# Performance work log

Hardware: AMD Instinct MI355X
Metric: run time of the kernel (lower is better)

The kernel has to match this reference:

```python
import jax, jax.numpy as jnp
import numpy as np

N_QUBITS = 4
DIM = 16
N_QLAYERS = 2

def _cnot_perm(c, t):
    idx = np.arange(DIM)
    cbit = (idx >> (N_QUBITS - 1 - c)) & 1
    return np.where(cbit == 1, idx ^ (1 << (N_QUBITS - 1 - t)), idx)

# ring entanglement: CNOT(0,1), CNOT(1,2), CNOT(2,3), CNOT(3,0)
RING_PERMS = [jnp.asarray(_cnot_perm(i, (i + 1) % N_QUBITS)) for i in range(N_QUBITS)]
_idx = np.arange(DIM)
ZSIGNS = jnp.asarray(np.stack([1.0 - 2.0 * ((_idx >> (N_QUBITS - 1 - q)) & 1) for q in range(N_QUBITS)], axis=1).astype(np.float32))  # (16, 4)

def _rx(t):
    c = jnp.cos(t / 2).astype(jnp.complex64)
    s = jnp.sin(t / 2).astype(jnp.complex64)
    return jnp.stack([jnp.stack([c, -1j * s]), jnp.stack([-1j * s, c])])

def _ry(t):
    c = jnp.cos(t / 2).astype(jnp.complex64)
    s = jnp.sin(t / 2).astype(jnp.complex64)
    return jnp.stack([jnp.stack([c, -s]), jnp.stack([s, c])])

def _rz(t):
    e = jnp.exp(-0.5j * t.astype(jnp.complex64))
    z = jnp.zeros((), jnp.complex64)
    return jnp.stack([jnp.stack([e, z]), jnp.stack([z, jnp.conj(e)])])

def _apply_1q(state, g, q):
    # wire 0 is the most significant bit (PennyLane convention)
    s = state.reshape(2 ** q, 2, 2 ** (N_QUBITS - 1 - q))
    return jnp.einsum('ij,ajc->aic', g, s).reshape(DIM)

def _circuit(angles, qw):
    # angles: (4,), qw: (n_qlayers, 4, 3); returns PauliZ expvals (4,)
    state = jnp.zeros(DIM, jnp.complex64).at[0].set(1.0)
    for q in range(N_QUBITS):
        state = _apply_1q(state, _ry(angles[q]), q)
    for l in range(N_QLAYERS):
        for q in range(N_QUBITS):
            state = _apply_1q(state, _rx(qw[l, q, 0]), q)
            state = _apply_1q(state, _ry(qw[l, q, 1]), q)
            state = _apply_1q(state, _rz(qw[l, q, 2]), q)
        for p in RING_PERMS:
            state = state[p]
    probs = jnp.abs(state) ** 2
    return probs @ ZSIGNS

def _conv(x, w, b, stride, pad):
    y = jax.lax.conv_general_dilated(x, w, (stride, stride), [(pad, pad), (pad, pad)], dimension_numbers=('NCHW', 'OIHW', 'NCHW'))
    return y + b[None, :, None, None]

def _bn(x, g, b, m, v):
    scale = (g / jnp.sqrt(v + 1e-5))[None, :, None, None]
    return (x - m[None, :, None, None]) * scale + b[None, :, None, None]

def _forward(x, c1w, c1b, bn1g, bn1b, bn1m, bn1v, c2w, c2b, bn2g, bn2b, bn2m, bn2v, c3w, c3b, bn3g, bn3b, bn3m, bn3v, pre_w, pre_b, qw, pw1, pb1, pw2, pb2):
    B = x.shape[0]
    h = jax.nn.relu(_bn(_conv(x, c1w, c1b, 4, 3), bn1g, bn1b, bn1m, bn1v))   # (B,32,56,56)
    h = jax.nn.relu(_bn(_conv(h, c2w, c2b, 2, 1), bn2g, bn2b, bn2m, bn2v))   # (B,64,28,28)
    h = jax.nn.relu(_bn(_conv(h, c3w, c3b, 2, 1), bn3g, bn3b, bn3m, bn3v))   # (B,128,14,14)
    h = h.reshape(B, 128, 2, 7, 2, 7).mean(axis=(3, 5))                       # AdaptiveAvgPool2d((2,2))
    f = h.reshape(B, 128 * 4)
    ang = jnp.tanh(f @ pre_w.T + pre_b) * jnp.pi                              # (B,4)
    qout = jax.vmap(lambda a: _circuit(a, qw))(ang)                            # (B,4) batched statevector sim
    h1 = jax.nn.relu(qout @ pw1.T + pb1)                                       # dropout inactive (eval)
    return h1 @ pw2.T + pb2

def setup_inputs() -> dict:
    key = jax.random.key(0)
    ks = jax.random.split(key, 16)
    d = {
        'x': jax.random.normal(ks[0], (128, 3, 224, 224), jnp.float32),
        'c1w': jax.random.normal(ks[1], (32, 3, 7, 7), jnp.float32) * 0.05,
        'c1b': jax.random.normal(ks[2], (32,), jnp.float32) * 0.05,
        'bn1g': jnp.ones((32,), jnp.float32), 'bn1b': jnp.zeros((32,), jnp.float32),
        'bn1m': jnp.zeros((32,), jnp.float32), 'bn1v': jnp.ones((32,), jnp.float32),
        'c2w': jax.random.normal(ks[3], (64, 32, 3, 3), jnp.float32) * 0.05,
        'c2b': jax.random.normal(ks[4], (64,), jnp.float32) * 0.05,
        'bn2g': jnp.ones((64,), jnp.float32), 'bn2b': jnp.zeros((64,), jnp.float32),
        'bn2m': jnp.zeros((64,), jnp.float32), 'bn2v': jnp.ones((64,), jnp.float32),
        'c3w': jax.random.normal(ks[5], (128, 64, 3, 3), jnp.float32) * 0.05,
        'c3b': jax.random.normal(ks[6], (128,), jnp.float32) * 0.05,
        'bn3g': jnp.ones((128,), jnp.float32), 'bn3b': jnp.zeros((128,), jnp.float32),
        'bn3m': jnp.zeros((128,), jnp.float32), 'bn3v': jnp.ones((128,), jnp.float32),
        'pre_w': jax.random.normal(ks[7], (4, 512), jnp.float32) * 0.04,
        'pre_b': jax.random.normal(ks[8], (4,), jnp.float32) * 0.04,
        'qw': jax.random.normal(ks[9], (2, 4, 3), jnp.float32) * 0.1,
        'pw1': jax.random.normal(ks[10], (64, 4), jnp.float32) * 0.5,
        'pb1': jax.random.normal(ks[11], (64,), jnp.float32) * 0.5,
        'pw2': jax.random.normal(ks[12], (5, 64), jnp.float32) * 0.12,
        'pb2': jax.random.normal(ks[13], (5,), jnp.float32) * 0.12,
    }
    return d

def reference(x, c1w, c1b, bn1g, bn1b, bn1m, bn1v, c2w, c2b, bn2g, bn2b, bn2m, bn2v, c3w, c3b, bn3g, bn3b, bn3m, bn3v, pre_w, pre_b, qw, pw1, pb1, pw2, pb2):
    return _forward(x, c1w, c1b, bn1g, bn1b, bn1m, bn1v, c2w, c2b, bn2g, bn2b, bn2m, bn2v, c3w, c3b, bn3g, bn3b, bn3m, bn3v, pre_w, pre_b, qw, pw1, pb1, pw2, pb2)
```

## Files before the change

### kernel.cpp

```cpp
#include <hip/hip_runtime.h>
#include <math.h>

#define DEV __device__ __forceinline__

typedef __attribute__((ext_vector_type(8))) __bf16 bf16x8;
typedef __attribute__((ext_vector_type(4))) float f32x4;

__global__ void prep_weights(
    const float* __restrict__ c1w, const float* __restrict__ c1b,
    const float* __restrict__ g1, const float* __restrict__ b1,
    const float* __restrict__ m1, const float* __restrict__ v1,
    const float* __restrict__ c2w, const float* __restrict__ c2b,
    const float* __restrict__ g2, const float* __restrict__ b2,
    const float* __restrict__ m2, const float* __restrict__ v2,
    const float* __restrict__ c3w, const float* __restrict__ c3b,
    const float* __restrict__ g3, const float* __restrict__ b3,
    const float* __restrict__ m3, const float* __restrict__ v3,
    __bf16* __restrict__ wb1, __bf16* __restrict__ wb2, __bf16* __restrict__ wb3,
    float* __restrict__ sc1, float* __restrict__ sh1,
    float* __restrict__ sc2, float* __restrict__ sh2,
    float* __restrict__ sc3, float* __restrict__ sh3)
{
    int gid = blockIdx.x * 256 + threadIdx.x;
    int gs = gridDim.x * 256;
    for (int e = gid; e < 32 * 192; e += gs) {
        int oc = e / 192, k = e % 192, rr = k >> 3, kw = k & 7;
        wb1[e] = (rr < 21 && kw >= 1) ? (__bf16)c1w[oc * 147 + rr * 7 + kw - 1]
                                      : (__bf16)0.f;
    }
    for (int e = gid; e < 64 * 384; e += gs) {
        int oc = e / 384, k = e % 384, rr = k >> 2, kw = k & 3;
        wb2[e] = (kw >= 1) ? (__bf16)c2w[oc * 288 + rr * 3 + kw - 1] : (__bf16)0.f;
    }
    for (int e = gid; e < 128 * 768; e += gs) {
        int oc = e / 768, k = e % 768, rr = k >> 2, kw = k & 3;
        wb3[e] = (kw >= 1) ? (__bf16)c3w[oc * 576 + rr * 3 + kw - 1] : (__bf16)0.f;
    }
    if (gid < 32) {
        float s = g1[gid] * rsqrtf(v1[gid] + 1e-5f);
        sc1[gid] = s; sh1[gid] = (c1b[gid] - m1[gid]) * s + b1[gid];
    } else if (gid < 96) {
        int i = gid - 32;
        float s = g2[i] * rsqrtf(v2[i] + 1e-5f);
        sc2[i] = s; sh2[i] = (c2b[i] - m2[i]) * s + b2[i];
    } else if (gid < 224) {
        int i = gid - 96;
        float s = g3[i] * rsqrtf(v3[i] + 1e-5f);
        sc3[i] = s; sh3[i] = (c3b[i] - m3[i]) * s + b3[i];
    }
}

__global__ __launch_bounds__(256, 3) void conv1_kernel(
    const float* __restrict__ x,
    const __bf16* __restrict__ wb,
    const float* __restrict__ scale, const float* __restrict__ shift,
    __bf16* __restrict__ out)
{
    constexpr int IHW = 224 * 224, OHW = 56 * 56, LDR = 72;
    __shared__ __attribute__((aligned(16))) __bf16 Is[256 * LDR];
    __shared__ __attribute__((aligned(16))) __bf16 Ws[32 * LDR];

    const int tid = threadIdx.x;
    const int sb0 = blockIdx.x * 256;
    const int sm = tid;

    int a_n, a_ih0, a_iw0;
    {
        int m = sb0 + sm;
        a_n = m / OHW;
        int rem = m % OHW;
        a_ih0 = (rem / 56) * 4 - 3;
        a_iw0 = (rem % 56) * 4 - 3;
    }
    unsigned ihok = 0;
    #pragma unroll
    for (int t = 0; t < 7; ++t)
        ihok |= (unsigned)(((a_ih0 + t) >= 0) && ((a_ih0 + t) < 224)) << t;
    const bool left = (a_iw0 < 0);
    const int boff = a_n * 3 * IHW + a_ih0 * 224 + (a_iw0 - 1);

    const int w_oc = tid >> 3, w_j = tid & 7;
    const int wave = tid >> 6, lane = tid & 63;
    const int quad = lane >> 4, l16 = lane & 15;

    f32x4 acc[2][4] = {};

    float4 RA[8], RB[8];
    bf16x8 wv;

    auto LOADI = [&](int ci) {
        #pragma unroll
        for (int r = 0; r < 8; ++r) {
            const int rr = ci * 8 + r;
            if (rr < 21) {
                const int ic = rr / 7, kh = rr % 7;
                int off = boff + (ic * IHW + kh * 224);
                int o0 = off < 0 ? 0 : off;
                int o1 = (off + 4) < 0 ? 0 : (off + 4);
                RA[r] = *(const float4*)(x + o0);
                RB[r] = *(const float4*)(x + o1);
            }
        }
        wv = *(const bf16x8*)&wb[(size_t)w_oc * 192 + ci * 64 + w_j * 8];
    };

    LOADI(0);

    #pragma unroll
    for (int ci = 0; ci < 3; ++ci) {
        __builtin_amdgcn_s_barrier();
        #pragma unroll
        for (int r = 0; r < 8; ++r) {
            const int rr = ci * 8 + r;
            bf16x8 h;
            if (rr >= 21) {
                h = (bf16x8){};
            } else {
                const int kh = rr % 7;
                float va[8] = {RA[r].x, RA[r].y, RA[r].z, RA[r].w,
                               RB[r].x, RB[r].y, RB[r].z, RB[r].w};
                bool rok = (ihok >> kh) & 1u;
                #pragma unroll
                for (int j = 0; j < 8; ++j) va[j] = rok ? va[j] : 0.f;
                #pragma unroll
                for (int j = 1; j <= 3; ++j) va[j] = left ? 0.f : va[j];
                #pragma unroll
                for (int j = 0; j < 8; ++j) h[j] = (__bf16)va[j];
            }
            *(bf16x8*)&Is[sm * LDR + r * 8] = h;
        }
        *(bf16x8*)&Ws[w_oc * LDR + w_j * 8] = wv;
        if (ci + 1 < 3) LOADI(ci + 1);
        asm volatile("s_waitcnt lgkmcnt(0)" ::: "memory");
        __builtin_amdgcn_s_barrier();

        #pragma unroll
        for (int kk = 0; kk < 2; ++kk) {
            bf16x8 afr[2], bfr[4];
            #pragma unroll
            for (int mt = 0; mt < 2; ++mt)
                afr[mt] = *(const bf16x8*)&Ws[(mt * 16 + l16) * LDR + kk * 32 + quad * 8];
            #pragma unroll
            for (int nt = 0; nt < 4; ++nt)
                bfr[nt] = *(const bf16x8*)&Is[(wave * 64 + nt * 16 + l16) * LDR + kk * 32 + quad * 8];
            #pragma unroll
            for (int mt = 0; mt < 2; ++mt)
                #pragma unroll
                for (int nt = 0; nt < 4; ++nt)
                    acc[mt][nt] = __builtin_amdgcn_mfma_f32_16x16x32_bf16(
                        afr[mt], bfr[nt], acc[mt][nt], 0, 0, 0);
        }
    }

    #pragma unroll
    for (int mt = 0; mt < 2; ++mt) {
        #pragma unroll
        for (int r = 0; r < 4; ++r) {
            int oc = mt * 16 + quad * 4 + r;
            float scl = scale[oc], shf = shift[oc];
            #pragma unroll
            for (int nt = 0; nt < 4; ++nt) {
                int sg = sb0 + wave * 64 + nt * 16 + l16;
                int n = sg / OHW, s = sg % OHW;
                float v = fmaf(acc[mt][nt][r], scl, shf);
                v = v > 0.f ? v : 0.f;
                out[((size_t)n * 32 + oc) * OHW + s] = (__bf16)v;
            }
        }
    }
}

template<int NOCT, int IC, int IH, int IW, int OH, int OW, int OC,
         int KTP, int KCH, int GXS>
DEV void conv_body64(
    const __bf16* __restrict__ xo,
    const __bf16* __restrict__ wb,
    const float* __restrict__ scale, const float* __restrict__ shift,
    __bf16* __restrict__ out, __bf16* Is, __bf16* Ws)
{
    constexpr int KS = 3, S = 2, P = 1;
    constexpr int KITER = KCH / 64;
    constexpr int OHW = OH * OW;
    constexpr int IHW = IH * IW;
    constexpr int LDR = 72;
    constexpr int WLD = NOCT / 2;

    const int tid = threadIdx.x;
    int bx = blockIdx.x;
    if (GXS > 0) bx = (bx & 7) * GXS + (bx >> 3);
    const int sb0 = bx * 256;
    const int oc0 = blockIdx.y * (NOCT * 16);

    const int sm = tid;
    int a_n, a_ih0, a_iw0;
    {
        int m = sb0 + sm;
        a_n = m / OHW;
        int rem = m % OHW;
        a_ih0 = (rem / OW) * S - P;
        a_iw0 = (rem % OW) * S - P;
    }
    unsigned ihok = 0;
    #pragma unroll
    for (int t = 0; t < KS; ++t)
        ihok |= (unsigned)(((a_ih0 + t) >= 0) && ((a_ih0 + t) < IH)) << t;
    const bool left = (a_iw0 < 0);
    const __bf16* xp = xo + ((size_t)a_n * IC * IHW + (ptrdiff_t)a_ih0 * IW
                             + (a_iw0 - 1));

    const int wave = tid >> 6, lane = tid & 63;
    const int quad = lane >> 4, l16 = lane & 15;

    f32x4 acc[NOCT][4] = {};

    unsigned Pu[32];
    bf16x8 wv[WLD];

    auto LOADI = [&](int ci) {
        const int k0 = ci * 64;
        #pragma unroll
        for (int r = 0; r < 16; ++r) {
            const int rr = (k0 / 4) + r;
            const int ic = rr / KS, kh = rr % KS;
            const unsigned* rp = (const unsigned*)(xp + (ic * IHW + kh * IW));
            Pu[r * 2]     = rp[0];
            Pu[r * 2 + 1] = rp[1];
        }
        #pragma unroll
        for (int i = 0; i < WLD; ++i) {
            int e = i * 256 + tid;
            wv[i] = *(const bf16x8*)&wb[(size_t)(oc0 + (e >> 3)) * KTP + k0 + (e & 7) * 8];
        }
    };

    LOADI(0);

    #pragma unroll
    for (int ci = 0; ci < KITER; ++ci) {
        __builtin_amdgcn_s_barrier();
        #pragma unroll
        for (int q = 0; q < 8; ++q) {
            union { unsigned u[4]; bf16x8 v; } tm;
            #pragma unroll
            for (int h = 0; h < 2; ++h) {
                const int r = 2 * q + h;
                const int kh = (ci * 16 + r) % KS;
                unsigned t0 = Pu[r * 2], t1 = Pu[r * 2 + 1];
                bool rok = (ihok >> kh) & 1u;
                t0 = rok ? t0 : 0u;
                t1 = rok ? t1 : 0u;
                t0 = left ? (t0 & 0x0000FFFFu) : t0;
                tm.u[h * 2]     = t0;
                tm.u[h * 2 + 1] = t1;
            }
            *(bf16x8*)&Is[sm * LDR + q * 8] = tm.v;
        }
        #pragma unroll
        for (int i = 0; i < WLD; ++i) {
            int e = i * 256 + tid;
            *(bf16x8*)&Ws[(e >> 3) * LDR + (e & 7) * 8] = wv[i];
        }
        if (ci + 1 < KITER) LOADI(ci + 1);
        asm volatile("s_waitcnt lgkmcnt(0)" ::: "memory");
        __builtin_amdgcn_s_barrier();

        #pragma unroll
        for (int kk = 0; kk < 2; ++kk) {
            bf16x8 afr[NOCT], bfr[4];
            #pragma unroll
            for (int mt = 0; mt < NOCT; ++mt)
                afr[mt] = *(const bf16x8*)&Ws[(mt * 16 + l16) * LDR + kk * 32 + quad * 8];
            #pragma unroll
            for (int nt = 0; nt < 4; ++nt)
                bfr[nt] = *(const bf16x8*)&Is[(wave * 64 + nt * 16 + l16) * LDR + kk * 32 + quad * 8];
            #pragma unroll
            for (int mt = 0; mt < NOCT; ++mt)
                #pragma unroll
                for (int nt = 0; nt < 4; ++nt)
                    acc[mt][nt] = __builtin_amdgcn_mfma_f32_16x16x32_bf16(
                        afr[mt], bfr[nt], acc[mt][nt], 0, 0, 0);
        }
    }

    #pragma unroll
    for (int mt = 0; mt < NOCT; ++mt) {
        #pragma unroll
        for (int r = 0; r < 4; ++r) {
            int oc = oc0 + mt * 16 + quad * 4 + r;
            float scl = scale[oc], shf = shift[oc];
            #pragma unroll
            for (int nt = 0; nt < 4; ++nt) {
                int sg = sb0 + wave * 64 + nt * 16 + l16;
                int n = sg / OHW, s = sg % OHW;
                float v = fmaf(acc[mt][nt][r], scl, shf);
                v = v > 0.f ? v : 0.f;
                out[((size_t)n * OC + oc) * OHW + s] = (__bf16)v;
            }
        }
    }
}

__global__ __launch_bounds__(256, 3) void conv2_kernel(
    const __bf16* __restrict__ xo, const __bf16* __restrict__ wb,
    const float* __restrict__ scale, const float* __restrict__ shift,
    __bf16* __restrict__ out)
{
    __shared__ __attribute__((aligned(16))) __bf16 Is[256 * 72];
    __shared__ __attribute__((aligned(16))) __bf16 Ws[64 * 72];
    conv_body64<4, 32, 56, 56, 28, 28, 64, 384, 384, 49>(
        xo, wb, scale, shift, out, Is, Ws);
}

__global__ __launch_bounds__(256, 3) void conv3_kernel(
    const __bf16* __restrict__ xo, const __bf16* __restrict__ wb,
    const float* __restrict__ scale, const float* __restrict__ shift,
    __bf16* __restrict__ out)
{
    __shared__ __attribute__((aligned(16))) __bf16 Is[256 * 72];
    __shared__ __attribute__((aligned(16))) __bf16 Ws[32 * 72];
    conv_body64<2, 64, 28, 28, 14, 14, 128, 768, 768, 0>(
        xo, wb, scale, shift, out, Is, Ws);
}

__global__ __launch_bounds__(256) void head_kernel(
    const __bf16* __restrict__ c3o,
    const float* __restrict__ pre_w, const float* __restrict__ pre_b,
    const float* __restrict__ qw,
    const float* __restrict__ pw1, const float* __restrict__ pb1,
    const float* __restrict__ pw2, const float* __restrict__ pb2,
    float* __restrict__ out)
{
    __shared__ __attribute__((aligned(16))) __bf16 slab[128 * 196];
    __shared__ float f[512];
    __shared__ float ang[4];
    __shared__ float zexp[4];
    __shared__ float h1[64];

    int b = blockIdx.x;
    int t = threadIdx.x;

    {
        const bf16x8* src = (const bf16x8*)(c3o + (size_t)b * 128 * 196);
        bf16x8* dst = (bf16x8*)slab;
        #pragma unroll
        for (int i = 0; i < 13; ++i) {
            int e = t + i * 256;
            if (e < 3136) dst[e] = src[e];
        }
    }
    __syncthreads();

    for (int p = t; p < 512; p += 256) {
        int c = p >> 2, i = (p >> 1) & 1, j = p & 1;
        int base = c * 196 + (i * 7) * 14 + j * 7;
        float s = 0.f;
        #pragma unroll
        for (int u = 0; u < 7; ++u)
            #pragma unroll
            for (int v = 0; v < 7; ++v)
                s += (float)slab[base + u * 14 + v];
        f[p] = s * (1.f / 49.f);
    }
    __syncthreads();

    int wv = t >> 6, lane = t & 63;
    float partial = 0.f;
    for (int d = lane; d < 512; d += 64)
        partial += f[d] * pre_w[wv * 512 + d];
    #pragma unroll
    for (int off = 32; off > 0; off >>= 1)
        partial += __shfl_down(partial, off, 64);
    if (lane == 0)
        ang[wv] = tanhf(partial + pre_b[wv]) * 3.14159265358979323846f;
    __syncthreads();

    if (t < 16) {
        const int i = t;
        float re = (i == 0) ? 1.f : 0.f;
        float im = 0.f;

        #pragma unroll
        for (int q = 0; q < 4; ++q) {
            const int m = 8 >> q;
            float th = ang[q] * 0.5f;
            float c = cosf(th), s = sinf(th);
            float pr = __shfl_xor(re, m, 64);
            float pi = __shfl_xor(im, m, 64);
            float ts = (i & m) ? s : -s;
            re = c * re + ts * pr;
            im = c * im + ts * pi;
        }
        #pragma unroll
        for (int l = 0; l < 2; ++l) {
            #pragma unroll
            for (int q = 0; q < 4; ++q) {
                const int m = 8 >> q;
                const float* qq = qw + (l * 4 + q) * 3;
                {
                    float th = qq[0] * 0.5f;
                    float c = cosf(th), s = sinf(th);
                    float pr = __shfl_xor(re, m, 64);
                    float pi = __shfl_xor(im, m, 64);
                    float rn = c * re + s * pi;
                    im = c * im - s * pr;
                    re = rn;
                }
                {
                    float th = qq[1] * 0.5f;
                    float c = cosf(th), s = sinf(th);
                    float pr = __shfl_xor(re, m, 64);
                    float pi = __shfl_xor(im, m, 64);
                    float ts = (i & m) ? s : -s;
                    re = c * re + ts * pr;
                    im = c * im + ts * pi;
                }
                {
                    float th = qq[2] * 0.5f;
                    float c = cosf(th), s = sinf(th);
                    float ts = (i & m) ? s : -s;
                    float rn = c * re - ts * im;
                    im = c * im + ts * re;
                    re = rn;
                }
            }
            #pragma unroll
            for (int e = 0; e < 4; ++e) {
                const int cm = 8 >> e, tm = 8 >> ((e + 1) & 3);
                float pr = __shfl_xor(re, tm, 64);
                float pi = __shfl_xor(im, tm, 64);
                bool sw = (i & cm) != 0;
                re = sw ? pr : re;
                im = sw ? pi : im;
            }
        }
        float p2 = re * re + im * im;
        #pragma unroll
        for (int q = 0; q < 4; ++q) {
            const int m = 8 >> q;
            float v = (i & m) ? -p2 : p2;
            v += __shfl_xor(v, 1, 64);
            v += __shfl_xor(v, 2, 64);
            v += __shfl_xor(v, 4, 64);
            v += __shfl_xor(v, 8, 64);
            if (i == 0) zexp[q] = v;
        }
    }
    __syncthreads();

    if (t < 64) {
        float s = pb1[t];
        #pragma unroll
        for (int k = 0; k < 4; ++k) s += zexp[k] * pw1[t * 4 + k];
        h1[t] = s > 0.f ? s : 0.f;
    }
    __syncthreads();

    if (t < 5) {
        float s = pb2[t];
        for (int k = 0; k < 64; ++k) s += h1[k] * pw2[t * 64 + k];
        out[b * 5 + t] = s;
    }
}

extern "C" void kernel_launch(void* const* d_in, const int* in_sizes, int n_in,
                              void* d_out, int out_size, void* d_ws, size_t ws_size,
                              hipStream_t stream) {
    const float* x    = (const float*)d_in[0];
    const float* c1w  = (const float*)d_in[1];
    const float* c1b  = (const float*)d_in[2];
    const float* bn1g = (const float*)d_in[3];
    const float* bn1b = (const float*)d_in[4];
    const float* bn1m = (const float*)d_in[5];
    const float* bn1v = (const float*)d_in[6];
    const float* c2w  = (const float*)d_in[7];
    const float* c2b  = (const float*)d_in[8];
    const float* bn2g = (const float*)d_in[9];
    const float* bn2b = (const float*)d_in[10];
    const float* bn2m = (const float*)d_in[11];
    const float* bn2v = (const float*)d_in[12];
    const float* c3w  = (const float*)d_in[13];
    const float* c3bi = (const float*)d_in[14];
    const float* bn3g = (const float*)d_in[15];
    const float* bn3b = (const float*)d_in[16];
    const float* bn3m = (const float*)d_in[17];
    const float* bn3v = (const float*)d_in[18];
    const float* prw  = (const float*)d_in[19];
    const float* prb  = (const float*)d_in[20];
    const float* qw   = (const float*)d_in[21];
    const float* pw1  = (const float*)d_in[22];
    const float* pb1  = (const float*)d_in[23];
    const float* pw2  = (const float*)d_in[24];
    const float* pb2  = (const float*)d_in[25];

    const int N = in_sizes[0] / (3 * 224 * 224);
    const size_t NC1 = (size_t)N * 32 * 56 * 56;
    const size_t NC2 = (size_t)N * 64 * 28 * 28;
    const size_t NC3 = (size_t)N * 128 * 14 * 14;

    __bf16* ws_h = (__bf16*)d_ws;
    __bf16* c1o = ws_h + 64;
    __bf16* c2o = ws_h + 64 + NC1 + 64 + 64;
    __bf16* c3o = ws_h + 64 + NC1 + 64 + 64 + NC2 + 64;
    __bf16* wb1 = c3o + NC3;
    __bf16* wb2 = wb1 + 32 * 192;
    __bf16* wb3 = wb2 + 64 * 384;
    float* sc1 = (float*)(wb3 + 128 * 768);
    float* sh1 = sc1 + 32;
    float* sc2 = sh1 + 32;  float* sh2 = sc2 + 64;
    float* sc3 = sh2 + 64;  float* sh3 = sc3 + 128;

    prep_weights<<<192, 256, 0, stream>>>(
        c1w, c1b, bn1g, bn1b, bn1m, bn1v,
        c2w, c2b, bn2g, bn2b, bn2m, bn2v,
        c3w, c3bi, bn3g, bn3b, bn3m, bn3v,
        wb1, wb2, wb3, sc1, sh1, sc2, sh2, sc3, sh3);

    conv1_kernel<<<dim3(401408 / 256, 1), 256, 0, stream>>>(x, wb1, sc1, sh1, c1o);
    conv2_kernel<<<dim3(100352 / 256, 1), 256, 0, stream>>>(c1o, wb2, sc2, sh2, c2o);
    conv3_kernel<<<dim3(25088 / 256, 4), 256, 0, stream>>>(c2o, wb3, sc3, sh3, c3o);
    head_kernel<<<N, 256, 0, stream>>>(c3o, prw, prb, qw,
                                       pw1, pb1, pw2, pb2, (float*)d_out);
}
```

Before: 231.6 us.

## Retile conv2/conv3 with smaller spatial blocks, cooperative row loads, and two-deep prefetch

The shared conv body is rewritten so each block covers fewer output positions (128 for conv2, 64 for conv3). Waves are split across output channels and spatial positions, and several threads share the im2col row loads for each position. Global loads are prefetched two K-steps ahead using alternating register sets, issued after the LDS barrier. The aim is more blocks for occupancy and more latency hiding, at the cost of extra weight reloads per block and more register pressure.

Measured after the change: 223.6 us. 3.5% less time.

```diff
diff --git a/kernel.cpp b/kernel.cpp
--- a/kernel.cpp
+++ b/kernel.cpp
@@ -170,9 +170,9 @@
     }
 }
 
-template<int NOCT, int IC, int IH, int IW, int OH, int OW, int OC,
-         int KTP, int KCH, int GXS>
-DEV void conv_body64(
+template<int SPB, int WSP, int IC, int IH, int IW, int OH, int OW, int OC,
+         int KCH, int GXS>
+DEV void conv_bodyB(
     const __bf16* __restrict__ xo,
     const __bf16* __restrict__ wb,
     const float* __restrict__ scale, const float* __restrict__ shift,
@@ -180,21 +180,25 @@
 {
     constexpr int KS = 3, S = 2, P = 1;
     constexpr int KITER = KCH / 64;
-    constexpr int OHW = OH * OW;
-    constexpr int IHW = IH * IW;
+    constexpr int OHW = OH * OW, IHW = IH * IW;
     constexpr int LDR = 72;
-    constexpr int WLD = NOCT / 2;
+    constexpr int TPS = 256 / SPB;
+    constexpr int RPT = 16 / TPS;
+    constexpr int WOC = 4 / WSP;
+    constexpr int WLD = (WOC * 32) / 32;
+    static_assert(KITER % 2 == 0, "double-buffer needs even KITER");
 
     const int tid = threadIdx.x;
     int bx = blockIdx.x;
     if (GXS > 0) bx = (bx & 7) * GXS + (bx >> 3);
-    const int sb0 = bx * 256;
-    const int oc0 = blockIdx.y * (NOCT * 16);
-
-    const int sm = tid;
+    const int sb0 = bx * SPB;
+
+    const int s_sp = tid & (SPB - 1);
+    const int gbase = (tid / SPB) * RPT;
+
     int a_n, a_ih0, a_iw0;
     {
-        int m = sb0 + sm;
+        int m = sb0 + s_sp;
         a_n = m / OHW;
         int rem = m % OHW;
         a_ih0 = (rem / OW) * S - P;
@@ -210,42 +214,43 @@
 
     const int wave = tid >> 6, lane = tid & 63;
     const int quad = lane >> 4, l16 = lane & 15;
-
-    f32x4 acc[NOCT][4] = {};
-
-    unsigned Pu[32];
-    bf16x8 wv[WLD];
-
-    auto LOADI = [&](int ci) {
+    const int woc = wave / WSP, wsp = wave - woc * WSP;
+
+    f32x4 acc[2][4] = {};
+
+    unsigned PuA[RPT * 2], PuB[RPT * 2];
+    bf16x8 wvA[WLD], wvB[WLD];
+
+    auto LOADI = [&](int ci, auto& Pu, auto& wv) {
         const int k0 = ci * 64;
         #pragma unroll
-        for (int r = 0; r < 16; ++r) {
-            const int rr = (k0 / 4) + r;
-            const int ic = rr / KS, kh = rr % KS;
-            const unsigned* rp = (const unsigned*)(xp + (ic * IHW + kh * IW));
-            Pu[r * 2]     = rp[0];
-            Pu[r * 2 + 1] = rp[1];
+        for (int j = 0; j < RPT; ++j) {
+            int rrr = ci * 16 + gbase + j;
+            unsigned ic = ((unsigned)rrr * 43691u) >> 17;
+            int kh = rrr - (int)ic * 3;
+            const unsigned* rp = (const unsigned*)(xp + ((int)ic * IHW + kh * IW));
+            Pu[j * 2]     = rp[0];
+            Pu[j * 2 + 1] = rp[1];
         }
         #pragma unroll
         for (int i = 0; i < WLD; ++i) {
             int e = i * 256 + tid;
-            wv[i] = *(const bf16x8*)&wb[(size_t)(oc0 + (e >> 3)) * KTP + k0 + (e & 7) * 8];
+            wv[i] = *(const bf16x8*)&wb[(size_t)(e >> 3) * KCH + k0 + (e & 7) * 8];
         }
     };
 
-    LOADI(0);
-
-    #pragma unroll
-    for (int ci = 0; ci < KITER; ++ci) {
+    auto STEP = [&](int ci, auto& Pu, auto& wv, auto& Pun, auto& wvn) {
         __builtin_amdgcn_s_barrier();
         #pragma unroll
-        for (int q = 0; q < 8; ++q) {
+        for (int q = 0; q < RPT / 2; ++q) {
             union { unsigned u[4]; bf16x8 v; } tm;
             #pragma unroll
             for (int h = 0; h < 2; ++h) {
-                const int r = 2 * q + h;
-                const int kh = (ci * 16 + r) % KS;
-                unsigned t0 = Pu[r * 2], t1 = Pu[r * 2 + 1];
+                const int j = 2 * q + h;
+                int rrr = ci * 16 + gbase + j;
+                unsigned icq = ((unsigned)rrr * 43691u) >> 17;
+                int kh = rrr - (int)icq * 3;
+                unsigned t0 = Pu[j * 2], t1 = Pu[j * 2 + 1];
                 bool rok = (ihok >> kh) & 1u;
                 t0 = rok ? t0 : 0u;
                 t1 = rok ? t1 : 0u;
@@ -253,44 +258,52 @@
                 tm.u[h * 2]     = t0;
                 tm.u[h * 2 + 1] = t1;
             }
-            *(bf16x8*)&Is[sm * LDR + q * 8] = tm.v;
+            *(bf16x8*)&Is[s_sp * LDR + (gbase + 2 * q) * 4] = tm.v;
         }
         #pragma unroll
         for (int i = 0; i < WLD; ++i) {
             int e = i * 256 + tid;
             *(bf16x8*)&Ws[(e >> 3) * LDR + (e & 7) * 8] = wv[i];
         }
-        if (ci + 1 < KITER) LOADI(ci + 1);
         asm volatile("s_waitcnt lgkmcnt(0)" ::: "memory");
         __builtin_amdgcn_s_barrier();
+        if (ci + 2 < KITER) LOADI(ci + 2, Pun, wvn);
 
         #pragma unroll
         for (int kk = 0; kk < 2; ++kk) {
-            bf16x8 afr[NOCT], bfr[4];
-            #pragma unroll
-            for (int mt = 0; mt < NOCT; ++mt)
-                afr[mt] = *(const bf16x8*)&Ws[(mt * 16 + l16) * LDR + kk * 32 + quad * 8];
+            bf16x8 afr[2], bfr[4];
+            #pragma unroll
+            for (int mt = 0; mt < 2; ++mt)
+                afr[mt] = *(const bf16x8*)&Ws[(woc * 32 + mt * 16 + l16) * LDR + kk * 32 + quad * 8];
             #pragma unroll
             for (int nt = 0; nt < 4; ++nt)
-                bfr[nt] = *(const bf16x8*)&Is[(wave * 64 + nt * 16 + l16) * LDR + kk * 32 + quad * 8];
-            #pragma unroll
-            for (int mt = 0; mt < NOCT; ++mt)
+                bfr[nt] = *(const bf16x8*)&Is[(wsp * 64 + nt * 16 + l16) * LDR + kk * 32 + quad * 8];
+            #pragma unroll
+            for (int mt = 0; mt < 2; ++mt)
                 #pragma unroll
                 for (int nt = 0; nt < 4; ++nt)
                     acc[mt][nt] = __builtin_amdgcn_mfma_f32_16x16x32_bf16(
                         afr[mt], bfr[nt], acc[mt][nt], 0, 0, 0);
         }
-    }
-
-    #pragma unroll
-    for (int mt = 0; mt < NOCT; ++mt) {
+    };
+
+    LOADI(0, PuA, wvA);
+    LOADI(1, PuB, wvB);
+    #pragma unroll
+    for (int cc = 0; cc < KITER; cc += 2) {
+        STEP(cc,     PuA, wvA, PuA, wvA);
+        STEP(cc + 1, PuB, wvB, PuB, wvB);
+    }
+
+    #pragma unroll
+    for (int mt = 0; mt < 2; ++mt) {
         #pragma unroll
         for (int r = 0; r < 4; ++r) {
-            int oc = oc0 + mt * 16 + quad * 4 + r;
+            int oc = woc * 32 + mt * 16 + quad * 4 + r;
             float scl = scale[oc], shf = shift[oc];
             #pragma unroll
             for (int nt = 0; nt < 4; ++nt) {
-                int sg = sb0 + wave * 64 + nt * 16 + l16;
+                int sg = sb0 + wsp * 64 + nt * 16 + l16;
                 int n = sg / OHW, s = sg % OHW;
                 float v = fmaf(acc[mt][nt][r], scl, shf);
                 v = v > 0.f ? v : 0.f;
@@ -305,9 +318,9 @@
     const float* __restrict__ scale, const float* __restrict__ shift,
     __bf16* __restrict__ out)
 {
-    __shared__ __attribute__((aligned(16))) __bf16 Is[256 * 72];
+    __shared__ __attribute__((aligned(16))) __bf16 Is[128 * 72];
     __shared__ __attribute__((aligned(16))) __bf16 Ws[64 * 72];
-    conv_body64<4, 32, 56, 56, 28, 28, 64, 384, 384, 49>(
+    conv_bodyB<128, 2, 32, 56, 56, 28, 28, 64, 384, 98>(
         xo, wb, scale, shift, out, Is, Ws);
 }
 
@@ -316,9 +329,9 @@
     const float* __restrict__ scale, const float* __restrict__ shift,
     __bf16* __restrict__ out)
 {
-    __shared__ __attribute__((aligned(16))) __bf16 Is[256 * 72];
-    __shared__ __attribute__((aligned(16))) __bf16 Ws[32 * 72];
-    conv_body64<2, 64, 28, 28, 14, 14, 128, 768, 768, 0>(
+    __shared__ __attribute__((aligned(16))) __bf16 Is[64 * 72];
+    __shared__ __attribute__((aligned(16))) __bf16 Ws[128 * 72];
+    conv_bodyB<64, 1, 64, 28, 28, 14, 14, 128, 768, 49>(
         xo, wb, scale, shift, out, Is, Ws);
 }
 
@@ -516,8 +529,8 @@
         wb1, wb2, wb3, sc1, sh1, sc2, sh2, sc3, sh3);
 
     conv1_kernel<<<dim3(401408 / 256, 1), 256, 0, stream>>>(x, wb1, sc1, sh1, c1o);
-    conv2_kernel<<<dim3(100352 / 256, 1), 256, 0, stream>>>(c1o, wb2, sc2, sh2, c2o);
-    conv3_kernel<<<dim3(25088 / 256, 4), 256, 0, stream>>>(c2o, wb3, sc3, sh3, c3o);
+    conv2_kernel<<<dim3(784, 1), 256, 0, stream>>>(c1o, wb2, sc2, sh2, c2o);
+    conv3_kernel<<<dim3(392, 1), 256, 0, stream>>>(c2o, wb3, sc3, sh3, c3o);
     head_kernel<<<N, 256, 0, stream>>>(c3o, prw, prb, qw,
                                        pw1, pb1, pw2, pb2, (float*)d_out);
 }
```
